# Optimization experiments

Hardware: AMD Instinct MI355X
Metric: run time of the kernel (lower is better)

Reference implementation:

```python
import jax, jax.numpy as jnp
import numpy as np

MAX_DEPTH = 8
LMBDA = 0.1
OUTPUT_DIM = 128


def setup_inputs() -> dict:
    key = jax.random.key(0)
    k1, k2, k3, k4, k5, k6 = jax.random.split(key, 6)
    B, D, C = 8192, 2048, OUTPUT_DIM
    n_inner = 2 ** MAX_DEPTH - 1  # 255 inner nodes, BFS order
    n_leaf = 2 ** MAX_DEPTH       # 256 leaves
    x = jax.random.normal(k1, (B, D), dtype=jnp.float32)
    target = jax.random.randint(k2, (B,), 0, C)
    # small scale so sigmoid gates are not saturated (log(pen), log(1-pen) finite)
    W = jax.random.normal(k3, (n_inner, D), dtype=jnp.float32) * 0.02
    b = jax.random.normal(k4, (n_inner,), dtype=jnp.float32) * 0.02
    beta = jax.random.normal(k5, (n_inner,), dtype=jnp.float32)
    leaf_params = jax.random.normal(k6, (n_leaf, C), dtype=jnp.float32)
    return {"x": x, "target": target, "W": W, "b": b, "beta": beta,
            "leaf_params": leaf_params}


def reference(x, target, W, b, beta, leaf_params):
    B = x.shape[0]
    C = leaf_params.shape[1]
    y = jax.nn.one_hot(target, C, dtype=x.dtype)  # target_onehot

    # All inner-node gates as one batched GEMM: p[b,i] = sigmoid(beta_i*(x@w_i+b_i))
    p = jax.nn.sigmoid(beta[None, :] * (x @ W.T + b[None, :]))  # [B, n_inner]

    # Level-by-level path probability propagation (BFS node order).
    path = jnp.ones((B, 1), x.dtype)
    penalties = []  # per-level [2^d] node penalties
    start = 0
    for d in range(MAX_DEPTH):
        n = 2 ** d
        p_lvl = p[:, start:start + n]                      # [B, 2^d]
        pen = jnp.sum(p_lvl * path, axis=0) / jnp.sum(path, axis=0)
        penalties.append(pen)
        # left child gets path*(1-p), right gets path*p; interleave -> next level
        path = jnp.stack([path * (1.0 - p_lvl), path * p_lvl], axis=-1).reshape(B, 2 * n)
        start += n
    # path: [B, n_leaf] leaf path probabilities (left-to-right order)

    Q = jax.nn.softmax(leaf_params, axis=-1)               # [n_leaf, C]
    TQ = y @ jnp.log(Q).T                                  # [B, n_leaf], y . log Q per leaf
    loss = jnp.mean(jnp.sum(path * TQ, axis=1))

    # Penalty C: only inner nodes whose children are NOT leaves contribute
    # (original get_penalty drops depth==max_depth nodes), depths 1..max_depth-1.
    Cpen = jnp.asarray(0.0, x.dtype)
    for d in range(MAX_DEPTH - 1):
        lam = LMBDA * 2.0 ** (-(d + 1))
        pen = penalties[d]
        Cpen = Cpen - lam * 0.5 * jnp.sum(jnp.log(pen) + jnp.log(1.0 - pen))

    total = -loss + Cpen

    # output: Q of the max-path-prob leaf per sample
    leaf_idx = jnp.argmax(path, axis=1)                    # [B]
    output = Q[leaf_idx]                                   # [B, C]
    return total, output
```

## Files before the change

### kernel.cpp

```cpp
#include <hip/hip_runtime.h>
#include <hip/hip_bf16.h>
#include <hip/hip_fp16.h>
#include <stdint.h>

#define B_SIZE 8192
#define D_SIZE 2048
#define C_SIZE 128
#define N_INNER 255
#define N_LEAF 256
#define NPAD 256
#define NBLK_PATH 512

typedef _Float16 half8 __attribute__((ext_vector_type(8)));
typedef __fp16 pk16x2 __attribute__((ext_vector_type(2)));
typedef float f32x4 __attribute__((ext_vector_type(4)));
typedef unsigned short u16;

__device__ inline uint32_t pkh(float a, float b) {
    pk16x2 h = __builtin_amdgcn_cvt_pkrtz(a, b);
    return __builtin_bit_cast(uint32_t, h);
}
__device__ inline void split4(const float4 v, uint2& hi, uint2& lo) {
    pk16x2 a01 = __builtin_amdgcn_cvt_pkrtz(v.x, v.y);
    pk16x2 a23 = __builtin_amdgcn_cvt_pkrtz(v.z, v.w);
    float r0 = v.x - (float)a01[0];
    float r1 = v.y - (float)a01[1];
    float r2 = v.z - (float)a23[0];
    float r3 = v.w - (float)a23[1];
    hi = make_uint2(__builtin_bit_cast(uint32_t, a01), __builtin_bit_cast(uint32_t, a23));
    lo = make_uint2(pkh(r0, r1), pkh(r2, r3));
}

__global__ __launch_bounds__(256) void prep_kernel(
    const float* __restrict__ Wsrc, u16* __restrict__ Wh, u16* __restrict__ Wl,
    const float* __restrict__ lp, float* __restrict__ Q, float* __restrict__ logQt)
{
    int bid = blockIdx.x;
    int t = threadIdx.x;
    if (bid < 256) {
        int row = bid;
        int k = t * 8;
        uint2 h0, l0, h1, l1;
        if (row < N_INNER) {
            float4 v0 = *(const float4*)(Wsrc + (size_t)row * D_SIZE + k);
            float4 v1 = *(const float4*)(Wsrc + (size_t)row * D_SIZE + k + 4);
            split4(v0, h0, l0); split4(v1, h1, l1);
        } else {
            h0 = l0 = h1 = l1 = make_uint2(0u, 0u);
        }
        *(uint2*)&Wh[(size_t)row * D_SIZE + k]     = h0;
        *(uint2*)&Wh[(size_t)row * D_SIZE + k + 4] = h1;
        *(uint2*)&Wl[(size_t)row * D_SIZE + k]     = l0;
        *(uint2*)&Wl[(size_t)row * D_SIZE + k + 4] = l1;
    } else {
        int row = bid - 256;
        __shared__ float red[128];
        float v = 0.f;
        if (t < 128) { v = lp[row * C_SIZE + t]; red[t] = v; }
        __syncthreads();
        for (int s = 64; s > 0; s >>= 1) { if (t < s) red[t] = fmaxf(red[t], red[t + s]); __syncthreads(); }
        float mx = red[0]; __syncthreads();
        float e = 0.f;
        if (t < 128) { e = expf(v - mx); red[t] = e; }
        __syncthreads();
        for (int s = 64; s > 0; s >>= 1) { if (t < s) red[t] += red[t + s]; __syncthreads(); }
        float sum = red[0];
        if (t < 128) {
            Q[row * C_SIZE + t] = e / sum;
            logQt[(size_t)t * N_LEAF + row] = (v - mx) - logf(sum);
        }
    }
}

#define GBM 64
#define GBK 32
#define GKSPLIT 4
#define KCHUNK (D_SIZE / GKSPLIT)
#define KITERS (KCHUNK / GBK)
#define LDKA 40

__global__ __launch_bounds__(256, 2) void gemm_mfma(
    const float* __restrict__ x, const u16* __restrict__ Wh, const u16* __restrict__ Wl,
    float* __restrict__ zp)
{
    __shared__ __align__(16) u16 sAh[4][GBM * LDKA];
    __shared__ __align__(16) u16 sAl[4][GBM * LDKA];

    const int t = threadIdx.x;
    const int lane = t & 63, w = t >> 6;
    const int lr = lane & 15, lq = lane >> 4;
    const int mi = blockIdx.x >> 2;
    const int kz = blockIdx.x & 3;
    const int m0 = mi * GBM;
    const int kb0 = kz * KCHUNK;

    f32x4 acc[4][4];
    #pragma unroll
    for (int mt = 0; mt < 4; ++mt)
        #pragma unroll
        for (int nt = 0; nt < 4; ++nt) acc[mt][nt] = (f32x4){0.f, 0.f, 0.f, 0.f};

    float4 av_c[8];
    #pragma unroll
    for (int i = 0; i < 8; ++i) {
        int idx = i * 64 + lane;
        int row = idx >> 3, ch = idx & 7;
        av_c[i] = *(const float4*)(x + (size_t)(m0 + row) * D_SIZE + kb0 + ch * 4);
    }
    half8 bh[4], bl[4];
    #pragma unroll
    for (int nt = 0; nt < 4; ++nt) {
        int row = w * 64 + nt * 16 + lr;
        bh[nt] = *(const half8*)(Wh + (size_t)row * D_SIZE + kb0 + lq * 8);
        bl[nt] = *(const half8*)(Wl + (size_t)row * D_SIZE + kb0 + lq * 8);
    }

    #pragma unroll
    for (int kt = 0; kt < KITERS; ++kt) {
        const int kb = kb0 + kt * GBK;
        half8 nbh[4], nbl[4];
        if (kt + 1 < KITERS) {
            #pragma unroll
            for (int nt = 0; nt < 4; ++nt) {
                int row = w * 64 + nt * 16 + lr;
                nbh[nt] = *(const half8*)(Wh + (size_t)row * D_SIZE + kb + GBK + lq * 8);
                nbl[nt] = *(const half8*)(Wl + (size_t)row * D_SIZE + kb + GBK + lq * 8);
            }
        }
        float4 av_n[8];
        if (kt + 1 < KITERS) {
            #pragma unroll
            for (int i = 0; i < 8; ++i) {
                int idx = i * 64 + lane;
                int row = idx >> 3, ch = idx & 7;
                av_n[i] = *(const float4*)(x + (size_t)(m0 + row) * D_SIZE + kb + GBK + ch * 4);
            }
        }
        #pragma unroll
        for (int i = 0; i < 8; ++i) {
            int idx = i * 64 + lane;
            int row = idx >> 3, ch = idx & 7;
            uint2 hi, lo; split4(av_c[i], hi, lo);
            *(uint2*)&sAh[w][row * LDKA + ch * 4] = hi;
            *(uint2*)&sAl[w][row * LDKA + ch * 4] = lo;
        }
        asm volatile("s_waitcnt lgkmcnt(0)" ::: "memory");
        half8 ah[4], al[4];
        #pragma unroll
        for (int mt = 0; mt < 4; ++mt) {
            int off = (mt * 16 + lr) * LDKA + lq * 8;
            ah[mt] = *(const half8*)&sAh[w][off];
            al[mt] = *(const half8*)&sAl[w][off];
        }
        #pragma unroll
        for (int mt = 0; mt < 4; ++mt)
            #pragma unroll
            for (int nt = 0; nt < 4; ++nt) {
                acc[mt][nt] = __builtin_amdgcn_mfma_f32_16x16x32_f16(ah[mt], bh[nt], acc[mt][nt], 0, 0, 0);
                acc[mt][nt] = __builtin_amdgcn_mfma_f32_16x16x32_f16(ah[mt], bl[nt], acc[mt][nt], 0, 0, 0);
                acc[mt][nt] = __builtin_amdgcn_mfma_f32_16x16x32_f16(al[mt], bh[nt], acc[mt][nt], 0, 0, 0);
            }
        if (kt + 1 < KITERS) {
            #pragma unroll
            for (int i = 0; i < 8; ++i) av_c[i] = av_n[i];
            #pragma unroll
            for (int nt = 0; nt < 4; ++nt) { bh[nt] = nbh[nt]; bl[nt] = nbl[nt]; }
        }
    }

    float* zout = zp + (size_t)kz * B_SIZE * NPAD;
    #pragma unroll
    for (int mt = 0; mt < 4; ++mt) {
        #pragma unroll
        for (int nt = 0; nt < 4; ++nt) {
            int gn = w * 64 + nt * 16 + lr;
            #pragma unroll
            for (int r = 0; r < 4; ++r) {
                int gm = m0 + mt * 16 + lq * 4 + r;
                zout[(size_t)gm * NPAD + gn] = acc[mt][nt][r];
            }
        }
    }
}

__global__ __launch_bounds__(256) void path_kernel(
    const float* __restrict__ z, const int* __restrict__ target,
    const float* __restrict__ bvec, const float* __restrict__ beta,
    const float* __restrict__ Q, const float* __restrict__ logQt,
    float* __restrict__ partial, float* __restrict__ out)
{
    __shared__ float pbuf[4][256];
    __shared__ float s_num[128], s_den[128], s_loss;
    const int t = threadIdx.x, w = t >> 6, lane = t & 63;
    const int c0 = lane * 4;
    float pnum[4] = {0.f, 0.f, 0.f, 0.f};
    float pden[4] = {0.f, 0.f, 0.f, 0.f};
    float loss = 0.f;

    if (t < 128) s_num[t] = 0.f;
    else s_den[t - 128] = 0.f;
    if (t == 0) s_loss = 0.f;
    __syncthreads();

    float bet[4], bia[4];
    #pragma unroll
    for (int j = 0; j < 4; ++j) {
        int c = c0 + j;
        bet[j] = (c < N_INNER) ? beta[c] : 0.f;
        bia[j] = (c < N_INNER) ? bvec[c] : 0.f;
    }

    for (int i = 0; i < 4; ++i) {
        int r = blockIdx.x * 16 + w * 4 + i;
        float4 s = make_float4(0.f, 0.f, 0.f, 0.f);
        #pragma unroll
        for (int p = 0; p < GKSPLIT; ++p) {
            float4 v = *(const float4*)(z + ((size_t)p * B_SIZE + r) * NPAD + c0);
            s.x += v.x; s.y += v.y; s.z += v.z; s.w += v.w;
        }
        float zv[4] = {s.x, s.y, s.z, s.w};
        float pv[4];
        #pragma unroll
        for (int j = 0; j < 4; ++j) {
            int c = c0 + j;
            pv[j] = (c < N_INNER) ? 1.f / (1.f + expf(-bet[j] * (zv[j] + bia[j]))) : 0.f;
        }
        *(float4*)&pbuf[w][c0] = make_float4(pv[0], pv[1], pv[2], pv[3]);
        asm volatile("s_waitcnt lgkmcnt(0)" ::: "memory");

        int tg = target[r];
        float4 lq4 = *(const float4*)(logQt + (size_t)tg * N_LEAF + c0);
        float lqa[4] = {lq4.x, lq4.y, lq4.z, lq4.w};
        float lsum = 0.f, bestV = -1.f;
        int bestI = 0;
        #pragma unroll
        for (int j = 0; j < 4; ++j) {
            int leaf = c0 + j;
            float pl = 1.f;
            #pragma unroll
            for (int d = 0; d < 8; ++d) {
                int node = (1 << d) - 1 + (leaf >> (8 - d));
                int bit = (leaf >> (7 - d)) & 1;
                float pvn = pbuf[w][node];
                pl *= bit ? pvn : (1.f - pvn);
            }
            lsum += pl * lqa[j];
            if (pl > bestV) { bestV = pl; bestI = leaf; }
        }
        if (lane < 32) {
            #pragma unroll
            for (int j = 0; j < 4; ++j) {
                int c = c0 + j;
                if (c < 127) {
                    int h = c + 1; int d = 31 - __clz(h);
                    float pp = 1.f;
                    for (int e = 0; e < d; ++e) {
                        int ha = h >> (d - e);
                        int bit = (h >> (d - 1 - e)) & 1;
                        float pvn = pbuf[w][ha - 1];
                        pp *= bit ? pvn : (1.f - pvn);
                    }
                    pnum[j] += pbuf[w][c] * pp;
                    pden[j] += pp;
                }
            }
        }
        #pragma unroll
        for (int m = 1; m < 64; m <<= 1) {
            lsum += __shfl_xor(lsum, m, 64);
            float ov = __shfl_xor(bestV, m, 64);
            int   oi = __shfl_xor(bestI, m, 64);
            if (ov > bestV || (ov == bestV && oi < bestI)) { bestV = ov; bestI = oi; }
        }
        loss += lsum;
        out[1 + (size_t)r * C_SIZE + lane]      = Q[bestI * C_SIZE + lane];
        out[1 + (size_t)r * C_SIZE + lane + 64] = Q[bestI * C_SIZE + lane + 64];
        asm volatile("" ::: "memory");
    }

    if (lane < 32) {
        #pragma unroll
        for (int j = 0; j < 4; ++j) {
            int c = c0 + j;
            if (c < 127) {
                atomicAdd(&s_num[c], pnum[j]);
                atomicAdd(&s_den[c], pden[j]);
            }
        }
    }
    if (lane == 0) atomicAdd(&s_loss, loss);
    __syncthreads();
    float* rec = partial + (size_t)blockIdx.x * 256;
    if (t < 127)        rec[t] = s_num[t];
    else if (t == 127)  rec[127] = s_loss;
    else if (t < 255)   rec[t] = s_den[t - 128];
    else                rec[255] = 0.f;
}

__global__ __launch_bounds__(256) void reduce_kernel(
    const float* __restrict__ partial, float* __restrict__ out)
{
    __shared__ float s[256];
    __shared__ float red[128];
    int t = threadIdx.x;
    float a0 = 0.f, a1 = 0.f, a2 = 0.f, a3 = 0.f;
    for (int r = 0; r < NBLK_PATH; r += 4) {
        a0 += partial[(size_t)(r + 0) * 256 + t];
        a1 += partial[(size_t)(r + 1) * 256 + t];
        a2 += partial[(size_t)(r + 2) * 256 + t];
        a3 += partial[(size_t)(r + 3) * 256 + t];
    }
    s[t] = (a0 + a1) + (a2 + a3);
    __syncthreads();
    float term = 0.f;
    if (t < 127) {
        int d = 31 - __clz(t + 1);
        float lam = 0.1f * exp2f(-(float)(d + 1));
        float pen = s[t] / s[128 + t];
        term = lam * 0.5f * (logf(pen) + logf(1.f - pen));
    }
    if (t < 128) { red[t] = term; }
    __syncthreads();
    for (int sh = 64; sh > 0; sh >>= 1) { if (t < sh) red[t] += red[t + sh]; __syncthreads(); }
    if (t == 0) out[0] = -(s[127] / (float)B_SIZE) - red[0];
}

extern "C" void kernel_launch(void* const* d_in, const int* in_sizes, int n_in,
                              void* d_out, int out_size, void* d_ws, size_t ws_size,
                              hipStream_t stream)
{
    const float* x    = (const float*)d_in[0];
    const int*   tgt  = (const int*)d_in[1];
    const float* W    = (const float*)d_in[2];
    const float* b    = (const float*)d_in[3];
    const float* beta = (const float*)d_in[4];
    const float* lp   = (const float*)d_in[5];
    float* out = (float*)d_out;

    float* z     = (float*)d_ws;
    float* Q     = z + (size_t)GKSPLIT * B_SIZE * NPAD;
    float* logQt = Q + (size_t)N_LEAF * C_SIZE;
    u16*   Wh    = (u16*)(logQt + (size_t)C_SIZE * N_LEAF);
    u16*   Wl    = Wh + (size_t)N_LEAF * D_SIZE;
    float* partial = (float*)(Wl + (size_t)N_LEAF * D_SIZE);

    prep_kernel<<<512, 256, 0, stream>>>(W, Wh, Wl, lp, Q, logQt);

    gemm_mfma<<<512, 256, 0, stream>>>(x, Wh, Wl, z);

    path_kernel<<<NBLK_PATH, 256, 0, stream>>>(
        z, tgt, b, beta, Q, logQt, partial, out);

    reduce_kernel<<<1, 256, 0, stream>>>(partial, out);
}
```

Baseline: 179.5 us.

## Split W to fp16 hi/lo inside GEMM, share path prefix products, widen reduce

```diff
diff --git a/kernel.cpp b/kernel.cpp
--- a/kernel.cpp
+++ b/kernel.cpp
@@ -30,45 +30,35 @@
     hi = make_uint2(__builtin_bit_cast(uint32_t, a01), __builtin_bit_cast(uint32_t, a23));
     lo = make_uint2(pkh(r0, r1), pkh(r2, r3));
 }
+__device__ inline void splitB8(const float4 v0, const float4 v1, half8& h, half8& l) {
+    uint2 h0, l0, h1, l1;
+    split4(v0, h0, l0);
+    split4(v1, h1, l1);
+    uint4 hh = make_uint4(h0.x, h0.y, h1.x, h1.y);
+    uint4 ll = make_uint4(l0.x, l0.y, l1.x, l1.y);
+    h = __builtin_bit_cast(half8, hh);
+    l = __builtin_bit_cast(half8, ll);
+}
 
 __global__ __launch_bounds__(256) void prep_kernel(
-    const float* __restrict__ Wsrc, u16* __restrict__ Wh, u16* __restrict__ Wl,
     const float* __restrict__ lp, float* __restrict__ Q, float* __restrict__ logQt)
 {
-    int bid = blockIdx.x;
+    int row = blockIdx.x;
     int t = threadIdx.x;
-    if (bid < 256) {
-        int row = bid;
-        int k = t * 8;
-        uint2 h0, l0, h1, l1;
-        if (row < N_INNER) {
-            float4 v0 = *(const float4*)(Wsrc + (size_t)row * D_SIZE + k);
-            float4 v1 = *(const float4*)(Wsrc + (size_t)row * D_SIZE + k + 4);
-            split4(v0, h0, l0); split4(v1, h1, l1);
-        } else {
-            h0 = l0 = h1 = l1 = make_uint2(0u, 0u);
-        }
-        *(uint2*)&Wh[(size_t)row * D_SIZE + k]     = h0;
-        *(uint2*)&Wh[(size_t)row * D_SIZE + k + 4] = h1;
-        *(uint2*)&Wl[(size_t)row * D_SIZE + k]     = l0;
-        *(uint2*)&Wl[(size_t)row * D_SIZE + k + 4] = l1;
-    } else {
-        int row = bid - 256;
-        __shared__ float red[128];
-        float v = 0.f;
-        if (t < 128) { v = lp[row * C_SIZE + t]; red[t] = v; }
-        __syncthreads();
-        for (int s = 64; s > 0; s >>= 1) { if (t < s) red[t] = fmaxf(red[t], red[t + s]); __syncthreads(); }
-        float mx = red[0]; __syncthreads();
-        float e = 0.f;
-        if (t < 128) { e = expf(v - mx); red[t] = e; }
-        __syncthreads();
-        for (int s = 64; s > 0; s >>= 1) { if (t < s) red[t] += red[t + s]; __syncthreads(); }
-        float sum = red[0];
-        if (t < 128) {
-            Q[row * C_SIZE + t] = e / sum;
-            logQt[(size_t)t * N_LEAF + row] = (v - mx) - logf(sum);
-        }
+    __shared__ float red[128];
+    float v = 0.f;
+    if (t < 128) { v = lp[row * C_SIZE + t]; red[t] = v; }
+    __syncthreads();
+    for (int s = 64; s > 0; s >>= 1) { if (t < s) red[t] = fmaxf(red[t], red[t + s]); __syncthreads(); }
+    float mx = red[0]; __syncthreads();
+    float e = 0.f;
+    if (t < 128) { e = expf(v - mx); red[t] = e; }
+    __syncthreads();
+    for (int s = 64; s > 0; s >>= 1) { if (t < s) red[t] += red[t + s]; __syncthreads(); }
+    float sum = red[0];
+    if (t < 128) {
+        Q[row * C_SIZE + t] = e / sum;
+        logQt[(size_t)t * N_LEAF + row] = (v - mx) - logf(sum);
     }
 }
 
@@ -80,7 +70,7 @@
 #define LDKA 40
 
 __global__ __launch_bounds__(256, 2) void gemm_mfma(
-    const float* __restrict__ x, const u16* __restrict__ Wh, const u16* __restrict__ Wl,
+    const float* __restrict__ x, const float* __restrict__ W,
     float* __restrict__ zp)
 {
     __shared__ __align__(16) u16 sAh[4][GBM * LDKA];
@@ -100,6 +90,13 @@
         #pragma unroll
         for (int nt = 0; nt < 4; ++nt) acc[mt][nt] = (f32x4){0.f, 0.f, 0.f, 0.f};
 
+    int brow[4];
+    #pragma unroll
+    for (int nt = 0; nt < 4; ++nt) {
+        int rrow = w * 64 + nt * 16 + lr;
+        brow[nt] = (rrow > 254) ? 254 : rrow;
+    }
+
     float4 av_c[8];
     #pragma unroll
     for (int i = 0; i < 8; ++i) {
@@ -110,21 +107,22 @@
     half8 bh[4], bl[4];
     #pragma unroll
     for (int nt = 0; nt < 4; ++nt) {
-        int row = w * 64 + nt * 16 + lr;
-        bh[nt] = *(const half8*)(Wh + (size_t)row * D_SIZE + kb0 + lq * 8);
-        bl[nt] = *(const half8*)(Wl + (size_t)row * D_SIZE + kb0 + lq * 8);
+        const float* p = W + (size_t)brow[nt] * D_SIZE + kb0 + lq * 8;
+        float4 b0 = *(const float4*)(p);
+        float4 b1 = *(const float4*)(p + 4);
+        splitB8(b0, b1, bh[nt], bl[nt]);
     }
 
     #pragma unroll
     for (int kt = 0; kt < KITERS; ++kt) {
         const int kb = kb0 + kt * GBK;
-        half8 nbh[4], nbl[4];
+        float4 nb0[4], nb1[4];
         if (kt + 1 < KITERS) {
             #pragma unroll
             for (int nt = 0; nt < 4; ++nt) {
-                int row = w * 64 + nt * 16 + lr;
-                nbh[nt] = *(const half8*)(Wh + (size_t)row * D_SIZE + kb + GBK + lq * 8);
-                nbl[nt] = *(const half8*)(Wl + (size_t)row * D_SIZE + kb + GBK + lq * 8);
+                const float* p = W + (size_t)brow[nt] * D_SIZE + kb + GBK + lq * 8;
+                nb0[nt] = *(const float4*)(p);
+                nb1[nt] = *(const float4*)(p + 4);
             }
         }
         float4 av_n[8];
@@ -164,7 +162,7 @@
             #pragma unroll
             for (int i = 0; i < 8; ++i) av_c[i] = av_n[i];
             #pragma unroll
-            for (int nt = 0; nt < 4; ++nt) { bh[nt] = nbh[nt]; bl[nt] = nbl[nt]; }
+            for (int nt = 0; nt < 4; ++nt) splitB8(nb0[nt], nb1[nt], bh[nt], bl[nt]);
         }
     }
 
@@ -231,21 +229,28 @@
         int tg = target[r];
         float4 lq4 = *(const float4*)(logQt + (size_t)tg * N_LEAF + c0);
         float lqa[4] = {lq4.x, lq4.y, lq4.z, lq4.w};
+
+        float P = 1.f;
+        #pragma unroll
+        for (int d = 0; d < 6; ++d) {
+            int node = (1 << d) - 1 + (c0 >> (8 - d));
+            int bit = (c0 >> (7 - d)) & 1;
+            float pvn = pbuf[w][node];
+            P *= bit ? pvn : (1.f - pvn);
+        }
+        float p6  = pbuf[w][63 + lane];
+        float p7a = pbuf[w][127 + 2 * lane];
+        float p7b = pbuf[w][127 + 2 * lane + 1];
         float lsum = 0.f, bestV = -1.f;
         int bestI = 0;
         #pragma unroll
         for (int j = 0; j < 4; ++j) {
-            int leaf = c0 + j;
-            float pl = 1.f;
-            #pragma unroll
-            for (int d = 0; d < 8; ++d) {
-                int node = (1 << d) - 1 + (leaf >> (8 - d));
-                int bit = (leaf >> (7 - d)) & 1;
-                float pvn = pbuf[w][node];
-                pl *= bit ? pvn : (1.f - pvn);
-            }
+            float t6 = (j & 2) ? p6 : (1.f - p6);
+            float p7 = (j & 2) ? p7b : p7a;
+            float t7 = (j & 1) ? p7 : (1.f - p7);
+            float pl = (P * t6) * t7;
             lsum += pl * lqa[j];
-            if (pl > bestV) { bestV = pl; bestI = leaf; }
+            if (pl > bestV) { bestV = pl; bestI = c0 + j; }
         }
         if (lane < 32) {
             #pragma unroll
@@ -297,20 +302,25 @@
     else                rec[255] = 0.f;
 }
 
-__global__ __launch_bounds__(256) void reduce_kernel(
+__global__ __launch_bounds__(1024) void reduce_kernel(
     const float* __restrict__ partial, float* __restrict__ out)
 {
+    __shared__ float part[4][256];
     __shared__ float s[256];
     __shared__ float red[128];
-    int t = threadIdx.x;
+    const int t = threadIdx.x;
+    const int col = t & 255, seg = t >> 8;
+    const int base = seg * (NBLK_PATH / 4);
     float a0 = 0.f, a1 = 0.f, a2 = 0.f, a3 = 0.f;
-    for (int r = 0; r < NBLK_PATH; r += 4) {
-        a0 += partial[(size_t)(r + 0) * 256 + t];
-        a1 += partial[(size_t)(r + 1) * 256 + t];
-        a2 += partial[(size_t)(r + 2) * 256 + t];
-        a3 += partial[(size_t)(r + 3) * 256 + t];
-    }
-    s[t] = (a0 + a1) + (a2 + a3);
+    for (int r = 0; r < NBLK_PATH / 4; r += 4) {
+        a0 += partial[(size_t)(base + r + 0) * 256 + col];
+        a1 += partial[(size_t)(base + r + 1) * 256 + col];
+        a2 += partial[(size_t)(base + r + 2) * 256 + col];
+        a3 += partial[(size_t)(base + r + 3) * 256 + col];
+    }
+    part[seg][col] = (a0 + a1) + (a2 + a3);
+    __syncthreads();
+    if (t < 256) s[t] = (part[0][t] + part[1][t]) + (part[2][t] + part[3][t]);
     __syncthreads();
     float term = 0.f;
     if (t < 127) {
@@ -337,19 +347,17 @@
     const float* lp   = (const float*)d_in[5];
     float* out = (float*)d_out;
 
-    float* z     = (float*)d_ws;
-    float* Q     = z + (size_t)GKSPLIT * B_SIZE * NPAD;
-    float* logQt = Q + (size_t)N_LEAF * C_SIZE;
-    u16*   Wh    = (u16*)(logQt + (size_t)C_SIZE * N_LEAF);
-    u16*   Wl    = Wh + (size_t)N_LEAF * D_SIZE;
-    float* partial = (float*)(Wl + (size_t)N_LEAF * D_SIZE);
-
-    prep_kernel<<<512, 256, 0, stream>>>(W, Wh, Wl, lp, Q, logQt);
-
-    gemm_mfma<<<512, 256, 0, stream>>>(x, Wh, Wl, z);
+    float* z       = (float*)d_ws;
+    float* Q       = z + (size_t)GKSPLIT * B_SIZE * NPAD;
+    float* logQt   = Q + (size_t)N_LEAF * C_SIZE;
+    float* partial = logQt + (size_t)C_SIZE * N_LEAF;
+
+    prep_kernel<<<256, 256, 0, stream>>>(lp, Q, logQt);
+
+    gemm_mfma<<<512, 256, 0, stream>>>(x, W, z);
 
     path_kernel<<<NBLK_PATH, 256, 0, stream>>>(
         z, tgt, b, beta, Q, logQt, partial, out);
 
-    reduce_kernel<<<1, 256, 0, stream>>>(partial, out);
-}
+    reduce_kernel<<<1, 1024, 0, stream>>>(partial, out);
+}
```

Result: faster. 168.1 us (-6.3%).
